# Performance work log

Hardware: AMD Instinct MI355X
Metric: run time of the kernel (lower is better)

Reference implementation:

```python
import jax, jax.numpy as jnp
import numpy as np

B, S, D, H = 1, 2048, 768, 12
HD = D // H


def layer_norm(x, g, b, eps=1e-5):
    mu = x.mean(-1, keepdims=True)
    var = ((x - mu) ** 2).mean(-1, keepdims=True)
    return (x - mu) * jax.lax.rsqrt(var + eps) * g + b


def setup_inputs() -> dict:
    key = jax.random.key(0)
    ks = jax.random.split(key, 16)
    s = 0.02
    exp_encodings = jax.random.normal(ks[0], (B, S, D), dtype=jnp.float32)
    pert_encodings = jax.random.normal(ks[1], (B, S, D), dtype=jnp.float32)
    adj = (jax.random.uniform(ks[2], (S, S)) < 0.01).astype(jnp.int32)
    adj = adj.at[jnp.arange(S), jnp.arange(S)].set(1)
    in_proj_w = jax.random.normal(ks[3], (3 * D, D)) * s
    in_proj_b = jnp.zeros((3 * D,), jnp.float32)
    out_proj_w = jax.random.normal(ks[4], (D, D)) * s
    out_proj_b = jnp.zeros((D,), jnp.float32)
    ln0_g = jnp.ones((D,), jnp.float32); ln0_b = jnp.zeros((D,), jnp.float32)
    ln1_g = jnp.ones((D,), jnp.float32); ln1_b = jnp.zeros((D,), jnp.float32)
    ln2_g = jnp.ones((D,), jnp.float32); ln2_b = jnp.zeros((D,), jnp.float32)
    w1 = jax.random.normal(ks[5], (D // 2, D)) * s
    b1 = jnp.zeros((D // 2,), jnp.float32)
    w2 = jax.random.normal(ks[6], (D, D // 2)) * s
    b2 = jnp.zeros((D,), jnp.float32)
    return dict(exp_encodings=exp_encodings, pert_encodings=pert_encodings,
                in_proj_w=in_proj_w, in_proj_b=in_proj_b,
                out_proj_w=out_proj_w, out_proj_b=out_proj_b,
                ln0_g=ln0_g, ln0_b=ln0_b, ln1_g=ln1_g, ln1_b=ln1_b,
                ln2_g=ln2_g, ln2_b=ln2_b, w1=w1, b1=b1, w2=w2, b2=b2,
                adj=adj)


def reference(exp_encodings, pert_encodings, in_proj_w, in_proj_b,
              out_proj_w, out_proj_b, ln0_g, ln0_b, ln1_g, ln1_b,
              ln2_g, ln2_b, w1, b1, w2, b2, adj):
    b, s, d = exp_encodings.shape
    hd = d // H
    # additive mask: 0 where edge, -inf elsewhere (diag guaranteed edge)
    mask = jnp.where(adj > 0, 0.0, -jnp.inf).astype(exp_encodings.dtype)
    x_in = layer_norm(exp_encodings + pert_encodings, ln0_g, ln0_b)
    # torch MultiheadAttention (batch_first) self-attention
    qkv = x_in @ in_proj_w.T + in_proj_b          # [b,s,3d]
    q, k, v = jnp.split(qkv, 3, axis=-1)
    q = q.reshape(b, s, H, hd)
    k = k.reshape(b, s, H, hd)
    v = v.reshape(b, s, H, hd)
    scores = jnp.einsum('bqhe,bkhe->bhqk', q, k) / np.sqrt(hd) + mask
    attn = jax.nn.softmax(scores, axis=-1)
    o = jnp.einsum('bhqk,bkhe->bqhe', attn, v).reshape(b, s, d)
    o = o @ out_proj_w.T + out_proj_b
    x = layer_norm(o + x_in, ln1_g, ln1_b)
    ff = jax.nn.relu(x @ w1.T + b1) @ w2.T + b2
    return layer_norm(x + ff, ln2_g, ln2_b)
```

## Files before the change

### kernel.cpp

```cpp
#include <hip/hip_runtime.h>

#define S 2048
#define D 768
#define NH 12
#define HD 64
#define TD (3 * D)

typedef __bf16 bf16_t;
typedef __bf16 v8bf __attribute__((ext_vector_type(8)));
typedef __bf16 v4bf __attribute__((ext_vector_type(4)));
typedef float v4f __attribute__((ext_vector_type(4)));

__device__ __forceinline__ float wave_reduce_sum(float v) {
#pragma unroll
    for (int o = 32; o > 0; o >>= 1) v += __shfl_down(v, o, 64);
    return v;
}
__device__ float block_reduce_sum(float v) {
    __shared__ float t4[4];
    int lane = threadIdx.x & 63, wid = threadIdx.x >> 6;
    v = wave_reduce_sum(v);
    __syncthreads();
    if (lane == 0) t4[wid] = v;
    __syncthreads();
    return t4[0] + t4[1] + t4[2] + t4[3];
}

template <int N>
__device__ __forceinline__ void wait_vmcnt() {
    if constexpr (N == 0) asm volatile("s_waitcnt vmcnt(0)" ::: "memory");
    else if constexpr (N == 1) asm volatile("s_waitcnt vmcnt(1)" ::: "memory");
    else if constexpr (N == 2) asm volatile("s_waitcnt vmcnt(2)" ::: "memory");
    else if constexpr (N == 3) asm volatile("s_waitcnt vmcnt(3)" ::: "memory");
    else if constexpr (N == 4) asm volatile("s_waitcnt vmcnt(4)" ::: "memory");
    else if constexpr (N == 5) asm volatile("s_waitcnt vmcnt(5)" ::: "memory");
    else if constexpr (N == 6) asm volatile("s_waitcnt vmcnt(6)" ::: "memory");
    else if constexpr (N == 7) asm volatile("s_waitcnt vmcnt(7)" ::: "memory");
    else asm volatile("s_waitcnt vmcnt(8)" ::: "memory");
}

#define NW0 (TD * D / 4)
#define NW1 (D * D / 4)
#define NW2 ((D / 2) * D / 4)
#define NW3 (D * (D / 2) / 4)
#define NWALL (NW0 + NW1 + NW2 + NW3)

__global__ __launch_bounds__(256) void addln_cvt(const float* __restrict__ A, const float* __restrict__ Bv,
                                                 const float* __restrict__ g, const float* __restrict__ be,
                                                 bf16_t* __restrict__ out,
                                                 const float* __restrict__ s0, const float* __restrict__ s1,
                                                 const float* __restrict__ s2, const float* __restrict__ s3,
                                                 bf16_t* __restrict__ d0, bf16_t* __restrict__ d1,
                                                 bf16_t* __restrict__ d2, bf16_t* __restrict__ d3) {
    int blk = blockIdx.x, t = threadIdx.x;
    if (blk >= S) {
        int i = (blk - S) * 256 + t;
        const float* sp; bf16_t* dp;
        if (i < NW0) { sp = s0; dp = d0; }
        else if (i < NW0 + NW1) { sp = s1; dp = d1; i -= NW0; }
        else if (i < NW0 + NW1 + NW2) { sp = s2; dp = d2; i -= NW0 + NW1; }
        else if (i < NWALL) { sp = s3; dp = d3; i -= NW0 + NW1 + NW2; }
        else return;
        float4 v = ((const float4*)sp)[i];
        v4bf o = {(bf16_t)v.x, (bf16_t)v.y, (bf16_t)v.z, (bf16_t)v.w};
        *(v4bf*)(dp + (size_t)i * 4) = o;
        return;
    }
    int row = blk;
    const float* a = A + (size_t)row * D;
    const float* b = Bv + (size_t)row * D;
    float x[3];
    float s = 0.f;
#pragma unroll
    for (int i = 0; i < 3; ++i) { int c = t + 256 * i; x[i] = a[c] + b[c]; s += x[i]; }
    float mean = block_reduce_sum(s) * (1.0f / D);
    float vs = 0.f;
#pragma unroll
    for (int i = 0; i < 3; ++i) { float d = x[i] - mean; vs += d * d; }
    float var = block_reduce_sum(vs) * (1.0f / D);
    float rstd = rsqrtf(var + 1e-5f);
#pragma unroll
    for (int i = 0; i < 3; ++i) {
        int c = t + 256 * i;
        out[(size_t)row * D + c] = (bf16_t)((x[i] - mean) * rstd * g[c] + be[c]);
    }
}

template <typename TO>
__global__ __launch_bounds__(256) void ln_only(const bf16_t* __restrict__ X,
                                               const float* __restrict__ g, const float* __restrict__ be,
                                               TO* __restrict__ out) {
    int row = blockIdx.x, t = threadIdx.x;
    const bf16_t* a = X + (size_t)row * D;
    float x[3];
    float s = 0.f;
#pragma unroll
    for (int i = 0; i < 3; ++i) { int c = t + 256 * i; x[i] = (float)a[c]; s += x[i]; }
    float mean = block_reduce_sum(s) * (1.0f / D);
    float vs = 0.f;
#pragma unroll
    for (int i = 0; i < 3; ++i) { float d = x[i] - mean; vs += d * d; }
    float var = block_reduce_sum(vs) * (1.0f / D);
    float rstd = rsqrtf(var + 1e-5f);
#pragma unroll
    for (int i = 0; i < 3; ++i) {
        int c = t + 256 * i;
        out[(size_t)row * D + c] = (TO)((x[i] - mean) * rstd * g[c] + be[c]);
    }
}

#define GBK 64

template <int TM, int TN, int RELU, bool RESID>
__global__ __launch_bounds__(256) void gemm_mfma(const bf16_t* __restrict__ A, const bf16_t* __restrict__ B,
                                                 const float* __restrict__ bias,
                                                 const bf16_t* __restrict__ Rsd, bf16_t* __restrict__ C,
                                                 int M, int N, int K) {
    constexpr int CA = TM * 8;
    constexpr int CHUNKS = (TM + TN) * 8;
    constexpr int P = CHUNKS / 256;
    static_assert(CHUNKS % 256 == 0, "chunk passes must be exact");
    constexpr int MI = TM / 32, NI = TN / 32;
    constexpr int BUFE = (TM + TN) * GBK;
    __shared__ bf16_t smem[2 * BUFE];
    const int t = threadIdx.x;
    const int lane = t & 63, wave = t >> 6;
    const int wr = (wave >> 1) * (TM / 2), wc = (wave & 1) * (TN / 2);
    const int m0 = blockIdx.y * TM, n0 = blockIdx.x * TN;
    const int lm = lane & 15, q = lane >> 4;

    const bf16_t* gp[P];
    int loff[P];
#pragma unroll
    for (int p = 0; p < P; ++p) {
        int c = t + 256 * p;
        if (c < CA) {
            int slab = c / (TM * 4), r4 = c % (TM * 4);
            gp[p] = A + (size_t)(m0 + (r4 >> 2)) * K + slab * 32 + (r4 & 3) * 8;
            loff[p] = slab * (TM * 32) + r4 * 8;
        } else {
            int cc = c - CA;
            int slab = cc / (TN * 4), r4 = cc % (TN * 4);
            gp[p] = B + (size_t)(n0 + (r4 >> 2)) * K + slab * 32 + (r4 & 3) * 8;
            loff[p] = TM * GBK + slab * (TN * 32) + r4 * 8;
        }
    }

    v4f acc[MI][NI] = {};

    auto stage = [&](int buf, int k0) {
#pragma unroll
        for (int p = 0; p < P; ++p)
            __builtin_amdgcn_global_load_lds(
                (const __attribute__((address_space(1))) void*)(gp[p] + k0),
                (__attribute__((address_space(3))) void*)(smem + buf * BUFE + loff[p]), 16, 0, 0);
    };

    stage(0, 0);
    int cur = 0;
    for (int k0 = 0; k0 < K; k0 += GBK) {
        if (k0 + GBK < K) {
            stage(cur ^ 1, k0 + GBK);
            __builtin_amdgcn_sched_barrier(0);
            wait_vmcnt<P>();
        } else {
            __builtin_amdgcn_sched_barrier(0);
            wait_vmcnt<0>();
        }
        __builtin_amdgcn_s_barrier();
        __builtin_amdgcn_sched_barrier(0);

        const bf16_t* As = smem + cur * BUFE;
        const bf16_t* Bs = As + TM * GBK;
        v8bf af[2][MI], bfr[2][NI];
#pragma unroll
        for (int s = 0; s < 2; ++s) {
#pragma unroll
            for (int i = 0; i < MI; ++i)
                af[s][i] = *(const v8bf*)(As + s * (TM * 32) + (wr + i * 16 + lm) * 32 + q * 8);
#pragma unroll
            for (int j = 0; j < NI; ++j)
                bfr[s][j] = *(const v8bf*)(Bs + s * (TN * 32) + (wc + j * 16 + lm) * 32 + q * 8);
        }
#pragma unroll
        for (int s = 0; s < 2; ++s)
#pragma unroll
            for (int i = 0; i < MI; ++i)
#pragma unroll
                for (int j = 0; j < NI; ++j)
                    acc[i][j] = __builtin_amdgcn_mfma_f32_16x16x32_bf16(af[s][i], bfr[s][j], acc[i][j], 0, 0, 0);
        __builtin_amdgcn_sched_barrier(0);
        __builtin_amdgcn_s_barrier();
        cur ^= 1;
    }

#pragma unroll
    for (int i = 0; i < MI; ++i)
#pragma unroll
        for (int j = 0; j < NI; ++j) {
            int col = n0 + wc + j * 16 + lm;
            float bs = bias[col];
#pragma unroll
            for (int r = 0; r < 4; ++r) {
                int row = m0 + wr + i * 16 + q * 4 + r;
                float v = acc[i][j][r] + bs;
                if (RELU) v = fmaxf(v, 0.f);
                if (RESID) v += (float)Rsd[(size_t)row * N + col];
                C[(size_t)row * N + col] = (bf16_t)v;
            }
        }
}

__global__ __launch_bounds__(256) void attn_sparse(const bf16_t* __restrict__ qkv, const int* __restrict__ adj,
                                                   bf16_t* __restrict__ O) {
    __shared__ int s_idx[128];
    __shared__ int s_cnt;
    __shared__ float s_q[D];
    __shared__ float s_p[NH][128];

    const int row = blockIdx.x, t = threadIdx.x;
    const int lane = t & 63, wave = t >> 6;
    if (t == 0) s_cnt = 0;
    __syncthreads();

    const int4* arow = (const int4*)(adj + (size_t)row * S);
#pragma unroll
    for (int p = 0; p < 2; ++p) {
        int4 v = arow[t + 256 * p];
        int base = (t + 256 * p) * 4;
        if (v.x) { int k = atomicAdd(&s_cnt, 1); if (k < 128) s_idx[k] = base + 0; }
        if (v.y) { int k = atomicAdd(&s_cnt, 1); if (k < 128) s_idx[k] = base + 1; }
        if (v.z) { int k = atomicAdd(&s_cnt, 1); if (k < 128) s_idx[k] = base + 2; }
        if (v.w) { int k = atomicAdd(&s_cnt, 1); if (k < 128) s_idx[k] = base + 3; }
    }
    for (int c = t; c < D; c += 256) s_q[c] = (float)qkv[(size_t)row * TD + c];
    __syncthreads();
    const int n = (s_cnt < 128) ? s_cnt : 128;

    for (int it = t; it < n * NH; it += 256) {
        int h = it / n, i = it - h * n;
        int j = s_idx[i];
        const bf16_t* kp = qkv + (size_t)j * TD + D + h * HD;
        const float* qp = s_q + h * HD;
        float dot = 0.f;
#pragma unroll
        for (int c = 0; c < HD; c += 8) {
            v8bf kv = *(const v8bf*)(kp + c);
#pragma unroll
            for (int e = 0; e < 8; ++e) dot += qp[c + e] * (float)kv[e];
        }
        s_p[h][i] = dot * 0.125f;
    }
    __syncthreads();

    for (int h = wave; h < NH; h += 4) {
        float v0 = (lane < n) ? s_p[h][lane] : -1e30f;
        float v1 = (lane + 64 < n) ? s_p[h][lane + 64] : -1e30f;
        float m = fmaxf(v0, v1);
#pragma unroll
        for (int o = 32; o > 0; o >>= 1) m = fmaxf(m, __shfl_xor(m, o, 64));
        float p0 = (lane < n) ? __expf(v0 - m) : 0.f;
        float p1 = (lane + 64 < n) ? __expf(v1 - m) : 0.f;
        float sm = p0 + p1;
#pragma unroll
        for (int o = 32; o > 0; o >>= 1) sm += __shfl_xor(sm, o, 64);
        float inv = 1.f / sm;
        if (lane < n) s_p[h][lane] = p0 * inv;
        if (lane + 64 < n) s_p[h][lane + 64] = p1 * inv;
    }
    __syncthreads();

    for (int o = t; o < D; o += 256) {
        int h = o >> 6, e = o & 63;
        const float* pp = s_p[h];
        float acc = 0.f;
        for (int i = 0; i < n; ++i)
            acc += pp[i] * (float)qkv[(size_t)s_idx[i] * TD + 2 * D + h * HD + e];
        O[(size_t)row * D + o] = (bf16_t)acc;
    }
}

extern "C" void kernel_launch(void* const* d_in, const int* in_sizes, int n_in,
                              void* d_out, int out_size, void* d_ws, size_t ws_size,
                              hipStream_t stream) {
    const float* exp_e = (const float*)d_in[0];
    const float* pert  = (const float*)d_in[1];
    const float* w_in  = (const float*)d_in[2];
    const float* b_in  = (const float*)d_in[3];
    const float* w_out = (const float*)d_in[4];
    const float* b_out = (const float*)d_in[5];
    const float* g0  = (const float*)d_in[6];
    const float* be0 = (const float*)d_in[7];
    const float* g1  = (const float*)d_in[8];
    const float* be1 = (const float*)d_in[9];
    const float* g2  = (const float*)d_in[10];
    const float* be2 = (const float*)d_in[11];
    const float* w1  = (const float*)d_in[12];
    const float* b1  = (const float*)d_in[13];
    const float* w2  = (const float*)d_in[14];
    const float* b2  = (const float*)d_in[15];
    const int*   adj = (const int*)d_in[16];
    float* out = (float*)d_out;

    const size_t SD = (size_t)S * D;
    bf16_t* wb_in  = (bf16_t*)d_ws;
    bf16_t* wb_out = wb_in + (size_t)TD * D;
    bf16_t* wb_1   = wb_out + (size_t)D * D;
    bf16_t* wb_2   = wb_1 + (size_t)(D / 2) * D;
    bf16_t* x_in   = wb_2 + (size_t)D * (D / 2);
    bf16_t* qkv    = x_in + SD;
    bf16_t* attn_o = qkv + 3 * SD;
    bf16_t* y1     = attn_o + SD;
    bf16_t* x1     = y1 + SD;
    bf16_t* ffh    = x1 + SD;
    bf16_t* y2     = ffh + SD / 2;

    const int CVTB = (NWALL + 255) / 256;
    addln_cvt<<<S + CVTB, 256, 0, stream>>>(exp_e, pert, g0, be0, x_in,
                                            w_in, w_out, w1, w2, wb_in, wb_out, wb_1, wb_2);
    gemm_mfma<64, 128, 0, false><<<dim3(TD / 128, S / 64), 256, 0, stream>>>(x_in, wb_in, b_in, nullptr, qkv, S, TD, D);
    attn_sparse<<<S, 256, 0, stream>>>(qkv, adj, attn_o);
    gemm_mfma<64, 64, 0, true><<<dim3(D / 64, S / 64), 256, 0, stream>>>(attn_o, wb_out, b_out, x_in, y1, S, D, D);
    ln_only<bf16_t><<<S, 256, 0, stream>>>(y1, g1, be1, x1);
    gemm_mfma<32, 64, 1, false><<<dim3((D / 2) / 64, S / 32), 256, 0, stream>>>(x1, wb_1, b1, nullptr, ffh, S, D / 2, D);
    gemm_mfma<64, 64, 0, true><<<dim3(D / 64, S / 64), 256, 0, stream>>>(ffh, wb_2, b2, x1, y2, S, D, D / 2);
    ln_only<float><<<S, 256, 0, stream>>>(y2, g2, be2, out);
}
```

Measured before the change: 188.7 us.

## Fuse LayerNorm into FF1 GEMM and run sparse attention one row per wave

Replaces the per-row sparse attention block with a wave-per-row kernel that compacts adjacency indices using ballot/popcount instead of shared atomics. It also accumulates all heads per lane in the PV step. Separately, LayerNorm1 is computed inside the FF1 GEMM prologue, which writes x1 from one column block and keeps the normalized A panel in shared memory. This removes a launch and a round-trip of y1/x1, at the cost of recomputing LN per column block and using large shared memory that limits occupancy.

```diff
diff --git a/kernel.cpp b/kernel.cpp
--- a/kernel.cpp
+++ b/kernel.cpp
@@ -5,6 +5,7 @@
 #define NH 12
 #define HD 64
 #define TD (3 * D)
+#define GBK 64
 
 typedef __bf16 bf16_t;
 typedef __bf16 v8bf __attribute__((ext_vector_type(8)));
@@ -14,6 +15,11 @@
 __device__ __forceinline__ float wave_reduce_sum(float v) {
 #pragma unroll
     for (int o = 32; o > 0; o >>= 1) v += __shfl_down(v, o, 64);
+    return v;
+}
+__device__ __forceinline__ float wave_allreduce_sum(float v) {
+#pragma unroll
+    for (int o = 32; o > 0; o >>= 1) v += __shfl_xor(v, o, 64);
     return v;
 }
 __device__ float block_reduce_sum(float v) {
@@ -109,8 +115,6 @@
     }
 }
 
-#define GBK 64
-
 template <int TM, int TN, int RELU, bool RESID>
 __global__ __launch_bounds__(256) void gemm_mfma(const bf16_t* __restrict__ A, const bf16_t* __restrict__ B,
                                                  const float* __restrict__ bias,
@@ -211,37 +215,172 @@
         }
 }
 
-__global__ __launch_bounds__(256) void attn_sparse(const bf16_t* __restrict__ qkv, const int* __restrict__ adj,
-                                                   bf16_t* __restrict__ O) {
-    __shared__ int s_idx[128];
-    __shared__ int s_cnt;
-    __shared__ float s_q[D];
-    __shared__ float s_p[NH][128];
-
-    const int row = blockIdx.x, t = threadIdx.x;
+#define FTM 32
+#define FTN 64
+__global__ __launch_bounds__(256) void ff1_fused(const bf16_t* __restrict__ Y1,
+                                                 const float* __restrict__ g, const float* __restrict__ be,
+                                                 const bf16_t* __restrict__ W1, const float* __restrict__ b1,
+                                                 bf16_t* __restrict__ X1, bf16_t* __restrict__ FFH) {
+    constexpr int K = D;
+    constexpr int NSLAB = K / 32;
+    constexpr int NOUT = D / 2;
+    constexpr int CB = FTN * 8;
+    constexpr int P = CB / 256;
+    constexpr int NI = FTN / 32;
+    __shared__ bf16_t Afull[NSLAB * FTM * 32];
+    __shared__ bf16_t Bs[2 * FTN * GBK];
+    const int t = threadIdx.x;
     const int lane = t & 63, wave = t >> 6;
-    if (t == 0) s_cnt = 0;
+    const int m0 = blockIdx.y * FTM, n0 = blockIdx.x * FTN;
+    const int lm = lane & 15, q = lane >> 4;
+
+    float ga0[8], bb0[8], ga1[8], bb1[8];
+#pragma unroll
+    for (int e = 0; e < 8; ++e) { ga0[e] = g[lane * 8 + e]; bb0[e] = be[lane * 8 + e]; }
+    if (lane < 32) {
+#pragma unroll
+        for (int e = 0; e < 8; ++e) { ga1[e] = g[(lane + 64) * 8 + e]; bb1[e] = be[(lane + 64) * 8 + e]; }
+    }
+    for (int rr = 0; rr < 8; ++rr) {
+        const int r = wave * 8 + rr, gr = m0 + r;
+        float xa[8], xb[8];
+        float s = 0.f;
+        v8bf ya = *(const v8bf*)(Y1 + (size_t)gr * D + lane * 8);
+#pragma unroll
+        for (int e = 0; e < 8; ++e) { xa[e] = (float)ya[e]; s += xa[e]; }
+        if (lane < 32) {
+            v8bf yb = *(const v8bf*)(Y1 + (size_t)gr * D + (lane + 64) * 8);
+#pragma unroll
+            for (int e = 0; e < 8; ++e) { xb[e] = (float)yb[e]; s += xb[e]; }
+        }
+        float mean = wave_allreduce_sum(s) * (1.0f / D);
+        float vs = 0.f;
+#pragma unroll
+        for (int e = 0; e < 8; ++e) { float d2 = xa[e] - mean; vs += d2 * d2; }
+        if (lane < 32) {
+#pragma unroll
+            for (int e = 0; e < 8; ++e) { float d2 = xb[e] - mean; vs += d2 * d2; }
+        }
+        float rstd = rsqrtf(wave_allreduce_sum(vs) * (1.0f / D) + 1e-5f);
+        v8bf oa;
+#pragma unroll
+        for (int e = 0; e < 8; ++e) oa[e] = (bf16_t)((xa[e] - mean) * rstd * ga0[e] + bb0[e]);
+        *(v8bf*)(Afull + (lane >> 2) * (FTM * 32) + r * 32 + (lane & 3) * 8) = oa;
+        if (blockIdx.x == 0) *(v8bf*)(X1 + (size_t)gr * D + lane * 8) = oa;
+        if (lane < 32) {
+            v8bf ob;
+#pragma unroll
+            for (int e = 0; e < 8; ++e) ob[e] = (bf16_t)((xb[e] - mean) * rstd * ga1[e] + bb1[e]);
+            const int ch = lane + 64;
+            *(v8bf*)(Afull + (ch >> 2) * (FTM * 32) + r * 32 + (ch & 3) * 8) = ob;
+            if (blockIdx.x == 0) *(v8bf*)(X1 + (size_t)gr * D + ch * 8) = ob;
+        }
+    }
+
+    const bf16_t* gp[P];
+    int loff[P];
+#pragma unroll
+    for (int p = 0; p < P; ++p) {
+        int c = t + 256 * p;
+        int slab = c / (FTN * 4), r4 = c % (FTN * 4);
+        gp[p] = W1 + (size_t)(n0 + (r4 >> 2)) * K + slab * 32 + (r4 & 3) * 8;
+        loff[p] = slab * (FTN * 32) + r4 * 8;
+    }
+    auto stageB = [&](int buf, int k0) {
+#pragma unroll
+        for (int p = 0; p < P; ++p)
+            __builtin_amdgcn_global_load_lds(
+                (const __attribute__((address_space(1))) void*)(gp[p] + k0),
+                (__attribute__((address_space(3))) void*)(Bs + buf * (FTN * GBK) + loff[p]), 16, 0, 0);
+    };
+    stageB(0, 0);
+    asm volatile("s_waitcnt lgkmcnt(0)" ::: "memory");
+    __builtin_amdgcn_s_barrier();
+
+    const int wr = (wave >> 1) * (FTM / 2);
+    const int wc = (wave & 1) * (FTN / 2);
+    v4f acc[NI] = {};
+    int cur = 0;
+    for (int k0 = 0; k0 < K; k0 += GBK) {
+        if (k0 + GBK < K) {
+            stageB(cur ^ 1, k0 + GBK);
+            __builtin_amdgcn_sched_barrier(0);
+            wait_vmcnt<P>();
+        } else {
+            __builtin_amdgcn_sched_barrier(0);
+            wait_vmcnt<0>();
+        }
+        __builtin_amdgcn_s_barrier();
+        __builtin_amdgcn_sched_barrier(0);
+
+        const bf16_t* BsC = Bs + cur * (FTN * GBK);
+        v8bf af[2], bfr[2][NI];
+#pragma unroll
+        for (int s = 0; s < 2; ++s) {
+            int slab = (k0 >> 5) + s;
+            af[s] = *(const v8bf*)(Afull + slab * (FTM * 32) + (wr + lm) * 32 + q * 8);
+#pragma unroll
+            for (int j = 0; j < NI; ++j)
+                bfr[s][j] = *(const v8bf*)(BsC + s * (FTN * 32) + (wc + j * 16 + lm) * 32 + q * 8);
+        }
+#pragma unroll
+        for (int s = 0; s < 2; ++s)
+#pragma unroll
+            for (int j = 0; j < NI; ++j)
+                acc[j] = __builtin_amdgcn_mfma_f32_16x16x32_bf16(af[s], bfr[s][j], acc[j], 0, 0, 0);
+        __builtin_amdgcn_sched_barrier(0);
+        __builtin_amdgcn_s_barrier();
+        cur ^= 1;
+    }
+
+#pragma unroll
+    for (int j = 0; j < NI; ++j) {
+        int col = n0 + wc + j * 16 + lm;
+        float bs = b1[col];
+#pragma unroll
+        for (int r = 0; r < 4; ++r) {
+            int row = m0 + wr + q * 4 + r;
+            float v = acc[j][r] + bs;
+            v = fmaxf(v, 0.f);
+            FFH[(size_t)row * NOUT + col] = (bf16_t)v;
+        }
+    }
+}
+
+__device__ void attn_row(int row, int lane, const bf16_t* __restrict__ qkv, const int* __restrict__ adj,
+                         bf16_t* __restrict__ O, int* __restrict__ widx,
+                         float* __restrict__ wq, float* __restrict__ wp) {
+    int cnt = 0;
+    const int4* arow = (const int4*)(adj + (size_t)row * S);
+    const unsigned long long lt = (1ull << lane) - 1;
+#pragma unroll
+    for (int p = 0; p < 8; ++p) {
+        int4 v = arow[lane + 64 * p];
+        int base = (lane + 64 * p) * 4;
+        int f[4] = {v.x, v.y, v.z, v.w};
+#pragma unroll
+        for (int c = 0; c < 4; ++c) {
+            unsigned long long m = __ballot(f[c] != 0);
+            if (f[c]) {
+                int k = cnt + (int)__popcll(m & lt);
+                if (k < 128) widx[k] = base + c;
+            }
+            cnt += (int)__popcll(m);
+        }
+    }
+    const int n = (cnt < 128) ? cnt : 128;
+
+    for (int ch = lane; ch < D / 8; ch += 64) {
+        v8bf qv = *(const v8bf*)(qkv + (size_t)row * TD + ch * 8);
+#pragma unroll
+        for (int e = 0; e < 8; ++e) wq[ch * 8 + e] = (float)qv[e];
+    }
     __syncthreads();
 
-    const int4* arow = (const int4*)(adj + (size_t)row * S);
-#pragma unroll
-    for (int p = 0; p < 2; ++p) {
-        int4 v = arow[t + 256 * p];
-        int base = (t + 256 * p) * 4;
-        if (v.x) { int k = atomicAdd(&s_cnt, 1); if (k < 128) s_idx[k] = base + 0; }
-        if (v.y) { int k = atomicAdd(&s_cnt, 1); if (k < 128) s_idx[k] = base + 1; }
-        if (v.z) { int k = atomicAdd(&s_cnt, 1); if (k < 128) s_idx[k] = base + 2; }
-        if (v.w) { int k = atomicAdd(&s_cnt, 1); if (k < 128) s_idx[k] = base + 3; }
-    }
-    for (int c = t; c < D; c += 256) s_q[c] = (float)qkv[(size_t)row * TD + c];
-    __syncthreads();
-    const int n = (s_cnt < 128) ? s_cnt : 128;
-
-    for (int it = t; it < n * NH; it += 256) {
+    for (int it = lane; it < n * NH; it += 64) {
         int h = it / n, i = it - h * n;
-        int j = s_idx[i];
-        const bf16_t* kp = qkv + (size_t)j * TD + D + h * HD;
-        const float* qp = s_q + h * HD;
+        const bf16_t* kp = qkv + (size_t)widx[i] * TD + D + h * HD;
+        const float* qp = wq + h * HD;
         float dot = 0.f;
 #pragma unroll
         for (int c = 0; c < HD; c += 8) {
@@ -249,13 +388,13 @@
 #pragma unroll
             for (int e = 0; e < 8; ++e) dot += qp[c + e] * (float)kv[e];
         }
-        s_p[h][i] = dot * 0.125f;
+        wp[h * 128 + i] = dot * 0.125f;
     }
     __syncthreads();
 
-    for (int h = wave; h < NH; h += 4) {
-        float v0 = (lane < n) ? s_p[h][lane] : -1e30f;
-        float v1 = (lane + 64 < n) ? s_p[h][lane + 64] : -1e30f;
+    for (int h = 0; h < NH; ++h) {
+        float v0 = (lane < n) ? wp[h * 128 + lane] : -1e30f;
+        float v1 = (lane + 64 < n) ? wp[h * 128 + lane + 64] : -1e30f;
         float m = fmaxf(v0, v1);
 #pragma unroll
         for (int o = 32; o > 0; o >>= 1) m = fmaxf(m, __shfl_xor(m, o, 64));
@@ -265,19 +404,30 @@
 #pragma unroll
         for (int o = 32; o > 0; o >>= 1) sm += __shfl_xor(sm, o, 64);
         float inv = 1.f / sm;
-        if (lane < n) s_p[h][lane] = p0 * inv;
-        if (lane + 64 < n) s_p[h][lane + 64] = p1 * inv;
+        if (lane < n) wp[h * 128 + lane] = p0 * inv;
+        if (lane + 64 < n) wp[h * 128 + lane + 64] = p1 * inv;
     }
     __syncthreads();
 
-    for (int o = t; o < D; o += 256) {
-        int h = o >> 6, e = o & 63;
-        const float* pp = s_p[h];
-        float acc = 0.f;
-        for (int i = 0; i < n; ++i)
-            acc += pp[i] * (float)qkv[(size_t)s_idx[i] * TD + 2 * D + h * HD + e];
-        O[(size_t)row * D + o] = (bf16_t)acc;
-    }
+    float acc[NH] = {};
+    for (int i = 0; i < n; ++i) {
+        const bf16_t* vp = qkv + (size_t)widx[i] * TD + 2 * D + lane;
+#pragma unroll
+        for (int j = 0; j < NH; ++j) acc[j] += wp[j * 128 + i] * (float)vp[j * HD];
+    }
+#pragma unroll
+    for (int j = 0; j < NH; ++j) O[(size_t)row * D + j * HD + lane] = (bf16_t)acc[j];
+}
+
+__global__ __launch_bounds__(256) void attn_sparse_w(const bf16_t* __restrict__ qkv,
+                                                     const int* __restrict__ adj,
+                                                     bf16_t* __restrict__ O) {
+    __shared__ int s_idx[4][128];
+    __shared__ float s_q[4][D];
+    __shared__ float s_p[4][NH * 128];
+    const int lane = threadIdx.x & 63, wave = threadIdx.x >> 6;
+    const int row = blockIdx.x * 4 + wave;
+    attn_row(row, lane, qkv, adj, O, s_idx[wave], s_q[wave], s_p[wave]);
 }
 
 extern "C" void kernel_launch(void* const* d_in, const int* in_sizes, int n_in,
@@ -319,10 +469,9 @@
     addln_cvt<<<S + CVTB, 256, 0, stream>>>(exp_e, pert, g0, be0, x_in,
                                             w_in, w_out, w1, w2, wb_in, wb_out, wb_1, wb_2);
     gemm_mfma<64, 128, 0, false><<<dim3(TD / 128, S / 64), 256, 0, stream>>>(x_in, wb_in, b_in, nullptr, qkv, S, TD, D);
-    attn_sparse<<<S, 256, 0, stream>>>(qkv, adj, attn_o);
+    attn_sparse_w<<<S / 4, 256, 0, stream>>>(qkv, adj, attn_o);
     gemm_mfma<64, 64, 0, true><<<dim3(D / 64, S / 64), 256, 0, stream>>>(attn_o, wb_out, b_out, x_in, y1, S, D, D);
-    ln_only<bf16_t><<<S, 256, 0, stream>>>(y1, g1, be1, x1);
-    gemm_mfma<32, 64, 1, false><<<dim3((D / 2) / 64, S / 32), 256, 0, stream>>>(x1, wb_1, b1, nullptr, ffh, S, D / 2, D);
+    ff1_fused<<<dim3((D / 2) / FTN, S / FTM), 256, 0, stream>>>(y1, g1, be1, wb_1, b1, x1, ffh);
     gemm_mfma<64, 64, 0, true><<<dim3(D / 64, S / 64), 256, 0, stream>>>(ffh, wb_2, b2, x1, y2, S, D, D / 2);
     ln_only<float><<<S, 256, 0, stream>>>(y2, g2, be2, out);
 }
```

New measurement: 191.2 us. No clear change (+1.3%).

## Precompute adjacency neighbor lists in prologue kernel and batch sparse attention PV loop

Applied to the files above, without the earlier changes.

Adjacency compaction moves out of the attention kernel into extra blocks of the first fused kernel. Those blocks use wave ballot and popcount, so neighbor order is deterministic and no shared atomics are needed. The attention kernel then reads precomputed index lists and counts, overlapping the scan with the LN/convert work instead of the QKV-dependent phase. The PV accumulation is restructured so each thread handles three heads with 8-wide batched loads over padded neighbor lists, giving more memory-level parallelism. It costs extra workspace and depends on CVTB_N being hardcoded to match the weight-conversion block count.

```diff
diff --git a/kernel.cpp b/kernel.cpp
--- a/kernel.cpp
+++ b/kernel.cpp
@@ -5,6 +5,7 @@
 #define NH 12
 #define HD 64
 #define TD (3 * D)
+#define GBK 64
 
 typedef __bf16 bf16_t;
 typedef __bf16 v8bf __attribute__((ext_vector_type(8)));
@@ -44,6 +45,8 @@
 #define NW2 ((D / 2) * D / 4)
 #define NW3 (D * (D / 2) / 4)
 #define NWALL (NW0 + NW1 + NW2 + NW3)
+#define CVTB_N 2880
+#define ADJB_N (S / 4)
 
 __global__ __launch_bounds__(256) void addln_cvt(const float* __restrict__ A, const float* __restrict__ Bv,
                                                  const float* __restrict__ g, const float* __restrict__ be,
@@ -51,8 +54,35 @@
                                                  const float* __restrict__ s0, const float* __restrict__ s1,
                                                  const float* __restrict__ s2, const float* __restrict__ s3,
                                                  bf16_t* __restrict__ d0, bf16_t* __restrict__ d1,
-                                                 bf16_t* __restrict__ d2, bf16_t* __restrict__ d3) {
+                                                 bf16_t* __restrict__ d2, bf16_t* __restrict__ d3,
+                                                 const int* __restrict__ adj,
+                                                 int* __restrict__ nbr_idx, int* __restrict__ nbr_cnt) {
     int blk = blockIdx.x, t = threadIdx.x;
+    if (blk >= S + CVTB_N) {
+        const int lane = t & 63, wave = t >> 6;
+        const int row = (blk - S - CVTB_N) * 4 + wave;
+        int cnt = 0;
+        const int4* arow = (const int4*)(adj + (size_t)row * S);
+        const unsigned long long lt = (1ull << lane) - 1;
+        int* dst = nbr_idx + (size_t)row * 128;
+#pragma unroll
+        for (int p = 0; p < 8; ++p) {
+            int4 v = arow[lane + 64 * p];
+            int base = (lane + 64 * p) * 4;
+            int f[4] = {v.x, v.y, v.z, v.w};
+#pragma unroll
+            for (int c = 0; c < 4; ++c) {
+                unsigned long long m = __ballot(f[c] != 0);
+                if (f[c]) {
+                    int k = cnt + (int)__popcll(m & lt);
+                    if (k < 128) dst[k] = base + c;
+                }
+                cnt += (int)__popcll(m);
+            }
+        }
+        if (lane == 0) nbr_cnt[row] = (cnt < 128) ? cnt : 128;
+        return;
+    }
     if (blk >= S) {
         int i = (blk - S) * 256 + t;
         const float* sp; bf16_t* dp;
@@ -108,8 +138,6 @@
         out[(size_t)row * D + c] = (TO)((x[i] - mean) * rstd * g[c] + be[c]);
     }
 }
-
-#define GBK 64
 
 template <int TM, int TN, int RELU, bool RESID>
 __global__ __launch_bounds__(256) void gemm_mfma(const bf16_t* __restrict__ A, const bf16_t* __restrict__ B,
@@ -211,45 +239,40 @@
         }
 }
 
-__global__ __launch_bounds__(256) void attn_sparse(const bf16_t* __restrict__ qkv, const int* __restrict__ adj,
+__global__ __launch_bounds__(256) void attn_sparse(const bf16_t* __restrict__ qkv,
+                                                   const int* __restrict__ nbr_idx,
+                                                   const int* __restrict__ nbr_cnt,
                                                    bf16_t* __restrict__ O) {
     __shared__ int s_idx[128];
-    __shared__ int s_cnt;
     __shared__ float s_q[D];
     __shared__ float s_p[NH][128];
 
     const int row = blockIdx.x, t = threadIdx.x;
     const int lane = t & 63, wave = t >> 6;
-    if (t == 0) s_cnt = 0;
-    __syncthreads();
-
-    const int4* arow = (const int4*)(adj + (size_t)row * S);
-#pragma unroll
-    for (int p = 0; p < 2; ++p) {
-        int4 v = arow[t + 256 * p];
-        int base = (t + 256 * p) * 4;
-        if (v.x) { int k = atomicAdd(&s_cnt, 1); if (k < 128) s_idx[k] = base + 0; }
-        if (v.y) { int k = atomicAdd(&s_cnt, 1); if (k < 128) s_idx[k] = base + 1; }
-        if (v.z) { int k = atomicAdd(&s_cnt, 1); if (k < 128) s_idx[k] = base + 2; }
-        if (v.w) { int k = atomicAdd(&s_cnt, 1); if (k < 128) s_idx[k] = base + 3; }
-    }
+    const int n = nbr_cnt[row];
+    const int npad = (n + 7) & ~7;
+
+    if (t < 128) s_idx[t] = (t < n) ? nbr_idx[(size_t)row * 128 + t] : row;
     for (int c = t; c < D; c += 256) s_q[c] = (float)qkv[(size_t)row * TD + c];
     __syncthreads();
-    const int n = (s_cnt < 128) ? s_cnt : 128;
-
-    for (int it = t; it < n * NH; it += 256) {
-        int h = it / n, i = it - h * n;
-        int j = s_idx[i];
-        const bf16_t* kp = qkv + (size_t)j * TD + D + h * HD;
-        const float* qp = s_q + h * HD;
-        float dot = 0.f;
-#pragma unroll
-        for (int c = 0; c < HD; c += 8) {
-            v8bf kv = *(const v8bf*)(kp + c);
-#pragma unroll
-            for (int e = 0; e < 8; ++e) dot += qp[c + e] * (float)kv[e];
-        }
-        s_p[h][i] = dot * 0.125f;
+
+    for (int it = t; it < npad * NH; it += 256) {
+        int h = it / npad, i = it - h * npad;
+        if (i < n) {
+            int j = s_idx[i];
+            const bf16_t* kp = qkv + (size_t)j * TD + D + h * HD;
+            const float* qp = s_q + h * HD;
+            float dot = 0.f;
+#pragma unroll
+            for (int c = 0; c < HD; c += 8) {
+                v8bf kv = *(const v8bf*)(kp + c);
+#pragma unroll
+                for (int e = 0; e < 8; ++e) dot += qp[c + e] * (float)kv[e];
+            }
+            s_p[h][i] = dot * 0.125f;
+        } else {
+            s_p[h][i] = 0.f;
+        }
     }
     __syncthreads();
 
@@ -270,14 +293,31 @@
     }
     __syncthreads();
 
-    for (int o = t; o < D; o += 256) {
-        int h = o >> 6, e = o & 63;
-        const float* pp = s_p[h];
-        float acc = 0.f;
-        for (int i = 0; i < n; ++i)
-            acc += pp[i] * (float)qkv[(size_t)s_idx[i] * TD + 2 * D + h * HD + e];
-        O[(size_t)row * D + o] = (bf16_t)acc;
-    }
+    const int h0 = t >> 6, e = t & 63;
+    const bf16_t* vbase = qkv + 2 * D + h0 * HD + e;
+    float a0 = 0.f, a1 = 0.f, a2 = 0.f;
+    for (int i = 0; i < npad; i += 8) {
+        float v0[8], v1[8], v2[8], p0[8], p1[8], p2[8];
+#pragma unroll
+        for (int k = 0; k < 8; ++k) {
+            const bf16_t* vp = vbase + (size_t)s_idx[i + k] * TD;
+            v0[k] = (float)vp[0];
+            v1[k] = (float)vp[256];
+            v2[k] = (float)vp[512];
+            p0[k] = s_p[h0][i + k];
+            p1[k] = s_p[h0 + 4][i + k];
+            p2[k] = s_p[h0 + 8][i + k];
+        }
+#pragma unroll
+        for (int k = 0; k < 8; ++k) {
+            a0 += p0[k] * v0[k];
+            a1 += p1[k] * v1[k];
+            a2 += p2[k] * v2[k];
+        }
+    }
+    O[(size_t)row * D + t] = (bf16_t)a0;
+    O[(size_t)row * D + t + 256] = (bf16_t)a1;
+    O[(size_t)row * D + t + 512] = (bf16_t)a2;
 }
 
 extern "C" void kernel_launch(void* const* d_in, const int* in_sizes, int n_in,
@@ -314,12 +354,14 @@
     bf16_t* x1     = y1 + SD;
     bf16_t* ffh    = x1 + SD;
     bf16_t* y2     = ffh + SD / 2;
-
-    const int CVTB = (NWALL + 255) / 256;
-    addln_cvt<<<S + CVTB, 256, 0, stream>>>(exp_e, pert, g0, be0, x_in,
-                                            w_in, w_out, w1, w2, wb_in, wb_out, wb_1, wb_2);
+    int* nbr_idx   = (int*)(y2 + SD);
+    int* nbr_cnt   = nbr_idx + (size_t)S * 128;
+
+    addln_cvt<<<S + CVTB_N + ADJB_N, 256, 0, stream>>>(exp_e, pert, g0, be0, x_in,
+                                                       w_in, w_out, w1, w2, wb_in, wb_out, wb_1, wb_2,
+                                                       adj, nbr_idx, nbr_cnt);
     gemm_mfma<64, 128, 0, false><<<dim3(TD / 128, S / 64), 256, 0, stream>>>(x_in, wb_in, b_in, nullptr, qkv, S, TD, D);
-    attn_sparse<<<S, 256, 0, stream>>>(qkv, adj, attn_o);
+    attn_sparse<<<S, 256, 0, stream>>>(qkv, nbr_idx, nbr_cnt, attn_o);
     gemm_mfma<64, 64, 0, true><<<dim3(D / 64, S / 64), 256, 0, stream>>>(attn_o, wb_out, b_out, x_in, y1, S, D, D);
     ln_only<bf16_t><<<S, 256, 0, stream>>>(y1, g1, be1, x1);
     gemm_mfma<32, 64, 1, false><<<dim3((D / 2) / 64, S / 32), 256, 0, stream>>>(x1, wb_1, b1, nullptr, ffh, S, D / 2, D);
```

Result: faster. 183.4 us (-2.8%).
